# Performance work log

Hardware: AMD Instinct MI355X
Metric: run time of the kernel (lower is better)

## Reference

```python
import jax, jax.numpy as jnp
import numpy as np

NEG = -9e15
ALPHA = 0.2  # leaky relu negative slope


def setup_inputs() -> dict:
    key = jax.random.key(0)
    k1, k2, k3, k4 = jax.random.split(key, 4)
    B, N, d = 8, 2048, 128
    h = jax.random.normal(k1, (B, N, d), dtype=jnp.float32)
    adj = jax.random.randint(k2, (B, N, N), 0, 2, dtype=jnp.int32)
    W = jax.random.normal(k3, (d, d), dtype=jnp.float32) * (1.414 / np.sqrt(d))
    a = jax.random.normal(k4, (2 * d, 1), dtype=jnp.float32) * 0.1
    return {"h": h, "adj": adj, "W": W, "a": a}


def reference(h, adj, W, a):
    d = W.shape[1]
    Wh = jnp.matmul(h, W)                       # [B, N, d]  (dropout p=0 -> identity)
    Wh1 = jnp.matmul(Wh, a[:d])                 # [B, N, 1]
    Wh2 = jnp.matmul(Wh, a[d:])                 # [B, N, 1]
    e = jax.nn.leaky_relu(Wh1 + jnp.swapaxes(Wh2, 1, 2), negative_slope=ALPHA)  # [B, N, N]
    scores = jnp.where(adj > 0, e, NEG)
    attention = jax.nn.softmax(scores, axis=-1)  # [B, N, N]
    h_prime = jnp.matmul(attention, Wh)          # [B, N, d]
    out = h + h_prime                            # residual=True, concat=False
    return out, attention
```

## Files before the change

### kernel.cpp

```cpp
#include <hip/hip_runtime.h>
#include <cstdint>
#include <cstddef>

typedef float  v4f __attribute__((ext_vector_type(4)));
typedef short  v8s __attribute__((ext_vector_type(8)));
typedef int    v4i __attribute__((ext_vector_type(4)));
typedef unsigned long long u64;

#define BB 8
#define NN 2048
#define DD 128
#define TI 16
#define NEGV (-9e15f)

__device__ __forceinline__ unsigned short f2bf(float x) {
  unsigned u = __float_as_uint(x);
  u = u + 0x7FFFu + ((u >> 16) & 1u);
  return (unsigned short)(u >> 16);
}

__device__ __forceinline__ unsigned cvt_pk_bf16(float lo, float hi) {
  unsigned r;
  asm("v_cvt_pk_bf16_f32 %0, %1, %2" : "=v"(r) : "v"(lo), "v"(hi));
  return r;
}

__global__ __launch_bounds__(256) void gat_k1(
    const float* __restrict__ h, const float* __restrict__ W, const float* __restrict__ a,
    short* __restrict__ whbT, float* __restrict__ wh1g, float* __restrict__ wh2g)
{
  __shared__ __align__(16) unsigned short wT[DD * 136];
  __shared__ __align__(16) unsigned short staging[DD * 72];

  const int tid  = threadIdx.x;
  const int lane = tid & 63;
  const int wid  = tid >> 6;
  const int m16  = lane & 15;
  const int quad = lane >> 4;
  const int b    = blockIdx.y;
  const int i0   = blockIdx.x * 64;

  {
    const v4f* W4 = (const v4f*)W;
    #pragma unroll
    for (int it = 0; it < 16; it++) {
      int idx = it * 256 + tid;
      int k  = idx >> 5;
      int c4 = (idx & 31) * 4;
      v4f wv = W4[idx];
      #pragma unroll
      for (int q = 0; q < 4; q++)
        wT[(c4 + q) * 136 + k] = f2bf(wv[q]);
    }
  }

  const float* hrow = h + (size_t)(b * NN + i0 + wid * 16 + m16) * DD;
  v8s af[4];
  #pragma unroll
  for (int ks = 0; ks < 4; ks++) {
    v4f x0 = *(const v4f*)(hrow + ks * 32 + quad * 8);
    v4f x1 = *(const v4f*)(hrow + ks * 32 + quad * 8 + 4);
    v8s t;
    t[0] = (short)f2bf(x0.x); t[1] = (short)f2bf(x0.y);
    t[2] = (short)f2bf(x0.z); t[3] = (short)f2bf(x0.w);
    t[4] = (short)f2bf(x1.x); t[5] = (short)f2bf(x1.y);
    t[6] = (short)f2bf(x1.z); t[7] = (short)f2bf(x1.w);
    af[ks] = t;
  }
  __syncthreads();

  v4f acc[8];
  #pragma unroll
  for (int t = 0; t < 8; t++) acc[t] = (v4f){0.f, 0.f, 0.f, 0.f};

  #pragma unroll
  for (int ks = 0; ks < 4; ks++) {
    #pragma unroll
    for (int t = 0; t < 8; t++) {
      v8s bf = *(const v8s*)&wT[(t * 16 + m16) * 136 + ks * 32 + quad * 8];
      acc[t] = __builtin_amdgcn_mfma_f32_16x16x32_bf16(af[ks], bf, acc[t], 0, 0, 0);
    }
  }

  {
    float a1v[8], a2v[8];
    #pragma unroll
    for (int t = 0; t < 8; t++) {
      a1v[t] = a[t * 16 + m16];
      a2v[t] = a[DD + t * 16 + m16];
    }
    #pragma unroll
    for (int r = 0; r < 4; r++) {
      float p1 = 0.f, p2 = 0.f;
      #pragma unroll
      for (int t = 0; t < 8; t++) {
        p1 += acc[t][r] * a1v[t];
        p2 += acc[t][r] * a2v[t];
      }
      #pragma unroll
      for (int off = 8; off > 0; off >>= 1) {
        p1 += __shfl_xor(p1, off);
        p2 += __shfl_xor(p2, off);
      }
      if (m16 == 0) {
        int gi = b * NN + i0 + wid * 16 + quad * 4 + r;
        wh1g[gi] = p1;
        wh2g[gi] = p2;
      }
    }
  }

  #pragma unroll
  for (int t = 0; t < 8; t++)
    #pragma unroll
    for (int r = 0; r < 4; r++)
      staging[(t * 16 + m16) * 72 + wid * 16 + quad * 4 + r] = f2bf(acc[t][r]);
  __syncthreads();

  #pragma unroll
  for (int it = 0; it < 4; it++) {
    int idx = it * 256 + tid;
    int c  = idx >> 3;
    int i8 = idx & 7;
    v8s val = *(const v8s*)&staging[c * 72 + i8 * 8];
    *(v8s*)(whbT + (size_t)b * DD * NN + (size_t)c * NN + i0 + i8 * 8) = val;
  }
}

__global__ __launch_bounds__(256) void gat_k0(
    const int* __restrict__ adj, const float* __restrict__ wh1g,
    const float* __restrict__ wh2g, unsigned* __restrict__ maskg,
    float* __restrict__ msg, float* __restrict__ rsg)
{
  const int tid  = threadIdx.x;
  const int lane = tid & 63;
  const int wid  = tid >> 6;
  const int b    = blockIdx.y;
  const int i    = blockIdx.x * 4 + wid;
  const size_t row = (size_t)b * NN + i;

  const v4i* arow = (const v4i*)(adj + row * NN);
  const v4f* w2   = (const v4f*)(wh2g + (size_t)b * NN);
  const float wh1v = wh1g[row];

  float e[32];
  float m = -INFINITY;
  unsigned mbits = 0u;
  #pragma unroll
  for (int u = 0; u < 8; u++) {
    v4i av  = __builtin_nontemporal_load(&arow[u * 64 + lane]);
    v4f w2v = w2[u * 64 + lane];
    #pragma unroll
    for (int q = 0; q < 4; q++) {
      bool mk = av[q] > 0;
      float x = wh1v + w2v[q];
      float ev = mk ? (x > 0.f ? x : 0.2f * x) : NEGV;
      e[u * 4 + q] = ev;
      m = fmaxf(m, ev);
      mbits |= (mk ? 1u : 0u) << (u * 4 + q);
    }
  }
  maskg[row * 64 + lane] = mbits;

  #pragma unroll
  for (int off = 32; off > 0; off >>= 1) m = fmaxf(m, __shfl_xor(m, off));
  float s = 0.f;
  #pragma unroll
  for (int k = 0; k < 32; k++) s += __expf(e[k] - m);
  #pragma unroll
  for (int off = 32; off > 0; off >>= 1) s += __shfl_xor(s, off);

  if (lane == 0) { msg[row] = m; rsg[row] = 1.f / s; }
}

__global__ __launch_bounds__(256, 4) void gat_k2(
    const float* __restrict__ h, const unsigned* __restrict__ maskg,
    const short* __restrict__ whbT, const float* __restrict__ wh1g,
    const float* __restrict__ wh2g, const float* __restrict__ msg,
    const float* __restrict__ rsg, float* __restrict__ out,
    float* __restrict__ attout)
{
  __shared__ __align__(16) float smem[4 * TI * DD];
  __shared__ unsigned masks[TI * 68];
  __shared__ float wh1s[TI], ms_s[TI], rs_s[TI];

  const int tid  = threadIdx.x;
  const int lane = tid & 63;
  const int wid  = tid >> 6;
  const int m16  = lane & 15;
  const int quad = lane >> 4;
  const int bid  = blockIdx.x;
  const int b    = bid & 7;
  const int i0   = (bid >> 3) * TI;

  float* wh2s = smem;
  unsigned short* atile = (unsigned short*)(smem + 2048) + wid * (TI * 68);

  {
    const v4f* w2g4 = (const v4f*)(wh2g + (size_t)b * NN);
    ((v4f*)wh2s)[tid]       = w2g4[tid];
    ((v4f*)wh2s)[tid + 256] = w2g4[tid + 256];
  }
  {
    const unsigned* mg = maskg + (size_t)(b * NN + i0) * 64;
    #pragma unroll
    for (int it = 0; it < 4; it++) {
      int idx = it * 256 + tid;
      masks[(idx >> 6) * 68 + (idx & 63)] = mg[idx];
    }
  }
  if (tid < TI) {
    wh1s[tid] = wh1g[b * NN + i0 + tid];
    ms_s[tid] = msg[b * NN + i0 + tid];
    rs_s[tid] = rsg[b * NN + i0 + tid];
  }
  __syncthreads();

  float wh1r[4], mir[4], rsr[4];
  #pragma unroll
  for (int it = 0; it < 4; it++) {
    wh1r[it] = wh1s[it * 4 + quad];
    mir[it]  = ms_s[it * 4 + quad];
    rsr[it]  = rs_s[it * 4 + quad];
  }

  const short* whbT_b = whbT + (size_t)b * DD * NN;
  float* attbase = attout + (size_t)(b * NN + i0) * NN;

  v4f acc[8];
  #pragma unroll
  for (int t = 0; t < 8; t++) acc[t] = (v4f){0.f, 0.f, 0.f, 0.f};

  for (int c = 0; c < 8; c++) {
    const int j0 = wid * 512 + c * 64;
    const int jb = j0 + quad * 8;

    v8s bfr0[8], bfr1[8];
    #pragma unroll
    for (int t = 0; t < 8; t++)
      bfr0[t] = *(const v8s*)(whbT_b + (size_t)(t * 16 + m16) * NN + jb);
    #pragma unroll
    for (int t = 0; t < 8; t++)
      bfr1[t] = *(const v8s*)(whbT_b + (size_t)(t * 16 + m16) * NN + jb + 32);

    const int ubit = (j0 >> 8) << 2;
    const int wq   = ((j0 >> 2) & 63) + m16;
    v4f w2v = ((const v4f*)wh2s)[(j0 >> 2) + m16];
    #pragma unroll
    for (int it = 0; it < 4; it++) {
      const int row = it * 4 + quad;
      unsigned mw = masks[row * 68 + wq];
      v4f at;
      #pragma unroll
      for (int q = 0; q < 4; q++) {
        float x = wh1r[it] + w2v[q];
        float ev = ((mw >> (ubit + q)) & 1u) ? (x > 0.f ? x : 0.2f * x) : NEGV;
        at[q] = __expf(ev - mir[it]) * rsr[it];
      }
      *(v4f*)(attbase + (size_t)row * NN + j0 + m16 * 4) = at;
      unsigned lo = cvt_pk_bf16(at[0], at[1]);
      unsigned hi = cvt_pk_bf16(at[2], at[3]);
      u64 dv = (u64)lo | ((u64)hi << 32);
      *(u64*)&atile[row * 68 + m16 * 4] = dv;
    }

    union { v8s s; u64 d[2]; } af0, af1;
    af0.d[0] = *(const u64*)&atile[m16 * 68 + quad * 8];
    af0.d[1] = *(const u64*)&atile[m16 * 68 + quad * 8 + 4];
    af1.d[0] = *(const u64*)&atile[m16 * 68 + 32 + quad * 8];
    af1.d[1] = *(const u64*)&atile[m16 * 68 + 32 + quad * 8 + 4];

    #pragma unroll
    for (int t = 0; t < 8; t++)
      acc[t] = __builtin_amdgcn_mfma_f32_16x16x32_bf16(af0.s, bfr0[t], acc[t], 0, 0, 0);
    #pragma unroll
    for (int t = 0; t < 8; t++)
      acc[t] = __builtin_amdgcn_mfma_f32_16x16x32_bf16(af1.s, bfr1[t], acc[t], 0, 0, 0);
  }

  __syncthreads();
  float* red = smem;
  #pragma unroll
  for (int t = 0; t < 8; t++)
    #pragma unroll
    for (int r = 0; r < 4; r++)
      red[wid * (TI * DD) + (quad * 4 + r) * DD + t * 16 + m16] = acc[t][r];
  __syncthreads();

  {
    const size_t base = (size_t)(b * NN + i0) * DD;
    #pragma unroll
    for (int it = 0; it < 2; it++) {
      int idx = it * 256 + tid;
      v4f s0 = ((const v4f*)red)[idx];
      v4f s1 = ((const v4f*)red)[idx + 512];
      v4f s2 = ((const v4f*)red)[idx + 1024];
      v4f s3 = ((const v4f*)red)[idx + 1536];
      v4f hv = *(const v4f*)(h + base + (size_t)idx * 4);
      v4f o  = hv + s0 + s1 + s2 + s3;
      *(v4f*)(out + base + (size_t)idx * 4) = o;
    }
  }
}

extern "C" void kernel_launch(void* const* d_in, const int* in_sizes, int n_in,
                              void* d_out, int out_size, void* d_ws, size_t ws_size,
                              hipStream_t stream) {
  const float* h  = (const float*)d_in[0];
  const int* adj  = (const int*)d_in[1];
  const float* W  = (const float*)d_in[2];
  const float* a  = (const float*)d_in[3];

  float* out    = (float*)d_out;
  float* attout = out + (size_t)BB * NN * DD;

  char* ws = (char*)d_ws;
  short* whbT = (short*)ws;                      ws += (size_t)BB * DD * NN * 2;
  float* wh1  = (float*)ws;                      ws += (size_t)BB * NN * 4;
  float* wh2  = (float*)ws;                      ws += (size_t)BB * NN * 4;
  float* msg  = (float*)ws;                      ws += (size_t)BB * NN * 4;
  float* rsg  = (float*)ws;                      ws += (size_t)BB * NN * 4;
  unsigned* maskg = (unsigned*)ws;

  gat_k1<<<dim3(NN / 64, BB), 256, 0, stream>>>(h, W, a, whbT, wh1, wh2);
  gat_k0<<<dim3(NN / 4, BB), 256, 0, stream>>>(adj, wh1, wh2, maskg, msg, rsg);
  gat_k2<<<dim3(NN / TI * BB), 256, 0, stream>>>(h, maskg, whbT, wh1, wh2, msg, rsg, out, attout);
}
```

Baseline: 289.1 us.

## Halve gat_k2 row tile to 8 rows, zero-padding MFMA A tile

The attention/aggregation kernel now processes 8 query rows per block instead of 16, doubling the grid. The bf16 A tile keeps 16 rows for the 16x16x32 MFMA, with the upper 8 rows zeroed once, and the LDS row stride changes from 68 to 72. The aim is more blocks for load balance and latency hiding, and less per-block exponential and store work. In exchange, each block re-streams the full Wh^T from global/L2 for half the useful rows, and half of every MFMA multiplies padding.

After: 361.2 us. 1.25x slower.

```diff
diff --git a/kernel.cpp b/kernel.cpp
--- a/kernel.cpp
+++ b/kernel.cpp
@@ -10,7 +10,7 @@
 #define BB 8
 #define NN 2048
 #define DD 128
-#define TI 16
+#define TR 8
 #define NEGV (-9e15f)
 
 __device__ __forceinline__ unsigned short f2bf(float x) {
@@ -180,9 +180,9 @@
     const float* __restrict__ rsg, float* __restrict__ out,
     float* __restrict__ attout)
 {
-  __shared__ __align__(16) float smem[4 * TI * DD];
-  __shared__ unsigned masks[TI * 68];
-  __shared__ float wh1s[TI], ms_s[TI], rs_s[TI];
+  __shared__ __align__(16) float smem[4352];
+  __shared__ unsigned masks[TR * 68];
+  __shared__ float wh1s[TR], ms_s[TR], rs_s[TR];
 
   const int tid  = threadIdx.x;
   const int lane = tid & 63;
@@ -191,10 +191,10 @@
   const int quad = lane >> 4;
   const int bid  = blockIdx.x;
   const int b    = bid & 7;
-  const int i0   = (bid >> 3) * TI;
+  const int i0   = (bid >> 3) * TR;
 
   float* wh2s = smem;
-  unsigned short* atile = (unsigned short*)(smem + 2048) + wid * (TI * 68);
+  unsigned short* atile = (unsigned short*)(smem + 2048) + wid * (16 * 72);
 
   {
     const v4f* w2g4 = (const v4f*)(wh2g + (size_t)b * NN);
@@ -204,21 +204,25 @@
   {
     const unsigned* mg = maskg + (size_t)(b * NN + i0) * 64;
     #pragma unroll
-    for (int it = 0; it < 4; it++) {
+    for (int it = 0; it < 2; it++) {
       int idx = it * 256 + tid;
       masks[(idx >> 6) * 68 + (idx & 63)] = mg[idx];
     }
   }
-  if (tid < TI) {
+  {
+    u64* az = (u64*)(atile + 8 * 72);
+    for (int idx = lane; idx < 144; idx += 64) az[idx] = 0ull;
+  }
+  if (tid < TR) {
     wh1s[tid] = wh1g[b * NN + i0 + tid];
     ms_s[tid] = msg[b * NN + i0 + tid];
     rs_s[tid] = rsg[b * NN + i0 + tid];
   }
   __syncthreads();
 
-  float wh1r[4], mir[4], rsr[4];
-  #pragma unroll
-  for (int it = 0; it < 4; it++) {
+  float wh1r[2], mir[2], rsr[2];
+  #pragma unroll
+  for (int it = 0; it < 2; it++) {
     wh1r[it] = wh1s[it * 4 + quad];
     mir[it]  = ms_s[it * 4 + quad];
     rsr[it]  = rs_s[it * 4 + quad];
@@ -247,7 +251,7 @@
     const int wq   = ((j0 >> 2) & 63) + m16;
     v4f w2v = ((const v4f*)wh2s)[(j0 >> 2) + m16];
     #pragma unroll
-    for (int it = 0; it < 4; it++) {
+    for (int it = 0; it < 2; it++) {
       const int row = it * 4 + quad;
       unsigned mw = masks[row * 68 + wq];
       v4f at;
@@ -261,14 +265,14 @@
       unsigned lo = cvt_pk_bf16(at[0], at[1]);
       unsigned hi = cvt_pk_bf16(at[2], at[3]);
       u64 dv = (u64)lo | ((u64)hi << 32);
-      *(u64*)&atile[row * 68 + m16 * 4] = dv;
+      *(u64*)&atile[row * 72 + m16 * 4] = dv;
     }
 
     union { v8s s; u64 d[2]; } af0, af1;
-    af0.d[0] = *(const u64*)&atile[m16 * 68 + quad * 8];
-    af0.d[1] = *(const u64*)&atile[m16 * 68 + quad * 8 + 4];
-    af1.d[0] = *(const u64*)&atile[m16 * 68 + 32 + quad * 8];
-    af1.d[1] = *(const u64*)&atile[m16 * 68 + 32 + quad * 8 + 4];
+    af0.d[0] = *(const u64*)&atile[m16 * 72 + quad * 8];
+    af0.d[1] = *(const u64*)&atile[m16 * 72 + quad * 8 + 4];
+    af1.d[0] = *(const u64*)&atile[m16 * 72 + 32 + quad * 8];
+    af1.d[1] = *(const u64*)&atile[m16 * 72 + 32 + quad * 8 + 4];
 
     #pragma unroll
     for (int t = 0; t < 8; t++)
@@ -280,26 +284,24 @@
 
   __syncthreads();
   float* red = smem;
-  #pragma unroll
-  for (int t = 0; t < 8; t++)
-    #pragma unroll
-    for (int r = 0; r < 4; r++)
-      red[wid * (TI * DD) + (quad * 4 + r) * DD + t * 16 + m16] = acc[t][r];
+  if (quad < 2) {
+    #pragma unroll
+    for (int t = 0; t < 8; t++)
+      #pragma unroll
+      for (int r = 0; r < 4; r++)
+        red[wid * (TR * DD) + (quad * 4 + r) * DD + t * 16 + m16] = acc[t][r];
+  }
   __syncthreads();
 
   {
     const size_t base = (size_t)(b * NN + i0) * DD;
-    #pragma unroll
-    for (int it = 0; it < 2; it++) {
-      int idx = it * 256 + tid;
-      v4f s0 = ((const v4f*)red)[idx];
-      v4f s1 = ((const v4f*)red)[idx + 512];
-      v4f s2 = ((const v4f*)red)[idx + 1024];
-      v4f s3 = ((const v4f*)red)[idx + 1536];
-      v4f hv = *(const v4f*)(h + base + (size_t)idx * 4);
-      v4f o  = hv + s0 + s1 + s2 + s3;
-      *(v4f*)(out + base + (size_t)idx * 4) = o;
-    }
+    v4f s0 = ((const v4f*)red)[tid];
+    v4f s1 = ((const v4f*)red)[tid + 256];
+    v4f s2 = ((const v4f*)red)[tid + 512];
+    v4f s3 = ((const v4f*)red)[tid + 768];
+    v4f hv = *(const v4f*)(h + base + (size_t)tid * 4);
+    v4f o  = hv + s0 + s1 + s2 + s3;
+    *(v4f*)(out + base + (size_t)tid * 4) = o;
   }
 }
 
@@ -324,5 +326,5 @@
 
   gat_k1<<<dim3(NN / 64, BB), 256, 0, stream>>>(h, W, a, whbT, wh1, wh2);
   gat_k0<<<dim3(NN / 4, BB), 256, 0, stream>>>(adj, wh1, wh2, maskg, msg, rsg);
-  gat_k2<<<dim3(NN / TI * BB), 256, 0, stream>>>(h, maskg, whbT, wh1, wh2, msg, rsg, out, attout);
-}
+  gat_k2<<<dim3(NN / TR * BB), 256, 0, stream>>>(h, maskg, whbT, wh1, wh2, msg, rsg, out, attout);
+}
```
